# Performance work log

Hardware: AMD Instinct MI355X
Metric: run time of the kernel (lower is better)

## Reference

```python
import jax, jax.numpy as jnp
import numpy as np

N, D = 65536, 64            # flattened batch, state dim (size_in)
G, K = 4, 512               # number of gammas, components per gamma


def setup_inputs() -> dict:
    key = jax.random.key(0)
    k1, k2 = jax.random.split(key)
    states = jax.random.normal(k1, (N, D), dtype=jnp.float32)
    centers = jax.random.normal(k2, (G, K, D), dtype=jnp.float32)  # RBF centers, one bank per gamma
    gammas = jnp.array([0.5, 1.0, 2.0, 5.0], dtype=jnp.float32)
    return {"states": states, "centers": centers, "gammas": gammas}


def reference(states, centers, gammas):
    # states: [N, D]; centers: [G, K, D]; gammas: [G]
    x2 = jnp.sum(states * states, axis=-1)            # [N]
    c2 = jnp.sum(centers * centers, axis=-1)          # [G, K]
    xc = jnp.einsum('nd,gkd->gnk', states, centers)   # [G, N, K]
    d2 = x2[None, :, None] + c2[:, None, :] - 2.0 * xc  # [G, N, K]
    d2 = jnp.maximum(d2, 0.0)
    feats = jnp.exp(-gammas[:, None, None] * d2)      # [G, N, K]
    # concatenate per-gamma feature banks along feature dim -> [N, G*K]
    out = jnp.moveaxis(feats, 0, 1).reshape(states.shape[0], -1)
    return out
```

## Files before the change

kernel.cpp:

```cpp
#include <hip/hip_runtime.h>
#include <math.h>

#define N_TOT 65536
#define D_DIM 64
#define G_NUM 4
#define K_NUM 512

typedef __attribute__((ext_vector_type(4))) float  f32x4;
typedef __attribute__((ext_vector_type(8))) short  short8;

typedef const __attribute__((address_space(1))) void glb_cv;
typedef __attribute__((address_space(3))) void lds_v;

__device__ __forceinline__ unsigned int f2u(float x)        { return __builtin_bit_cast(unsigned int, x); }
__device__ __forceinline__ float        u2f(unsigned int x) { return __builtin_bit_cast(float, x); }

__device__ __forceinline__ unsigned int bf_rne(float x) {
    unsigned int u = f2u(x);
    return (u + 0x7FFFu + ((u >> 16) & 1u)) >> 16;
}

__device__ __forceinline__ int swz(int row, int byteInRow) {
    return (row << 7) + (byteInRow ^ ((row & 7) << 4));
}

#define AHI_OFF 0
#define ALO_OFF 16384
#define BHI_OFF 32768
#define BLO_OFF 49152

__global__ void prep_kernel(const float* __restrict__ in,
                            unsigned char* __restrict__ tiles,
                            float* __restrict__ sq, int nrows)
{
    int gtid = blockIdx.x * 256 + threadIdx.x;
    if (gtid >= nrows * 8) return;
    int row = gtid >> 3, c = gtid & 7;
    const float* p = in + (size_t)row * D_DIM + 8 * c;
    float4 v0 = *(const float4*)p;
    float4 v1 = *(const float4*)(p + 4);
    float vs[8] = {v0.x, v0.y, v0.z, v0.w, v1.x, v1.y, v1.z, v1.w};
    unsigned hi[4], lo[4];
    float s = 0.f;
    #pragma unroll
    for (int i = 0; i < 4; ++i) {
        float a = vs[2 * i], b = vs[2 * i + 1];
        s += a * a + b * b;
        unsigned ha = f2u(a) & 0xFFFF0000u, hb = f2u(b) & 0xFFFF0000u;
        hi[i] = (ha >> 16) | hb;
        lo[i] = bf_rne(a - u2f(ha)) | (bf_rne(b - u2f(hb)) << 16);
    }
    int tile = row >> 7, r = row & 127;
    int cs = c ^ (r & 7);
    unsigned char* base = tiles + (size_t)tile * 32768 + r * 128 + cs * 16;
    *(uint4*)(base)         = make_uint4(hi[0], hi[1], hi[2], hi[3]);
    *(uint4*)(base + 16384) = make_uint4(lo[0], lo[1], lo[2], lo[3]);
    s += __shfl_xor(s, 1, 64);
    s += __shfl_xor(s, 2, 64);
    s += __shfl_xor(s, 4, 64);
    if (c == 0) sq[row] = s;
}

__global__ __launch_bounds__(256, 2)
void rbf_mfma2(const unsigned char* __restrict__ Aprep,
               const unsigned char* __restrict__ Bprep,
               const float* __restrict__ gammas,
               const float* __restrict__ x2,
               const float* __restrict__ c2,
               float* __restrict__ out)
{
    __shared__ __align__(16) unsigned char lds[65536];

    const int tid = threadIdx.x;
    const int n0  = blockIdx.x * 128;
    const int kt  = blockIdx.y;
    const int g   = blockIdx.z;
    const int k0  = kt * 128;

    const int lane = tid & 63;
    const int w    = tid >> 6;

    const unsigned char* Asrc = Aprep + (size_t)blockIdx.x * 32768;
    const unsigned char* Bsrc = Bprep + (size_t)(g * 4 + kt) * 32768;
    #pragma unroll
    for (int i = 0; i < 8; ++i) {
        const int off = w * 8192 + i * 1024;
        __builtin_amdgcn_global_load_lds((glb_cv*)(Asrc + off + lane * 16),
                                         (lds_v*)(lds + off), 16, 0, 0);
        __builtin_amdgcn_global_load_lds((glb_cv*)(Bsrc + off + lane * 16),
                                         (lds_v*)(lds + 32768 + off), 16, 0, 0);
    }
    __syncthreads();

    const int wr = w >> 1;
    const int wc = w & 1;
    const int fr = lane & 15;
    const int q  = lane >> 4;

    short8 xhi[4][2], xlo[4][2];
    #pragma unroll
    for (int ms = 0; ms < 4; ++ms) {
        const int row = wr * 64 + ms * 16 + fr;
        #pragma unroll
        for (int h = 0; h < 2; ++h) {
            const int off = swz(row, 64 * h + 16 * q);
            xhi[ms][h] = *(const short8*)(lds + AHI_OFF + off);
            xlo[ms][h] = *(const short8*)(lds + ALO_OFF + off);
        }
    }

    f32x4 acc[4][4];
    #pragma unroll
    for (int ms = 0; ms < 4; ++ms)
        #pragma unroll
        for (int ns = 0; ns < 4; ++ns)
            acc[ms][ns] = (f32x4){0.f, 0.f, 0.f, 0.f};

    #pragma unroll
    for (int ns = 0; ns < 4; ++ns) {
        const int rowc = wc * 64 + ns * 16 + fr;
        short8 chi[2], clo[2];
        #pragma unroll
        for (int h = 0; h < 2; ++h) {
            const int off = swz(rowc, 64 * h + 16 * q);
            chi[h] = *(const short8*)(lds + BHI_OFF + off);
            clo[h] = *(const short8*)(lds + BLO_OFF + off);
        }
        #pragma unroll
        for (int ms = 0; ms < 4; ++ms) {
            #pragma unroll
            for (int h = 0; h < 2; ++h) {
                acc[ms][ns] = __builtin_amdgcn_mfma_f32_16x16x32_bf16(chi[h], xhi[ms][h], acc[ms][ns], 0, 0, 0);
                acc[ms][ns] = __builtin_amdgcn_mfma_f32_16x16x32_bf16(chi[h], xlo[ms][h], acc[ms][ns], 0, 0, 0);
                acc[ms][ns] = __builtin_amdgcn_mfma_f32_16x16x32_bf16(clo[h], xhi[ms][h], acc[ms][ns], 0, 0, 0);
            }
        }
    }

    const float gamma = gammas[g];

    float c2v[4][4];
    const float* c2g = c2 + g * K_NUM + k0 + wc * 64;
    #pragma unroll
    for (int ns = 0; ns < 4; ++ns) {
        float4 t = *(const float4*)(c2g + ns * 16 + 4 * q);
        c2v[ns][0] = t.x; c2v[ns][1] = t.y; c2v[ns][2] = t.z; c2v[ns][3] = t.w;
    }

    #pragma unroll
    for (int ms = 0; ms < 4; ++ms) {
        const int n = n0 + wr * 64 + ms * 16 + fr;
        const float xv = x2[n];
        float* rowp = out + (size_t)n * (G_NUM * K_NUM) + (size_t)g * K_NUM + k0 + wc * 64;
        #pragma unroll
        for (int ns = 0; ns < 4; ++ns) {
            float4 o;
            o.x = __expf(-gamma * fmaxf(xv + c2v[ns][0] - 2.0f * acc[ms][ns][0], 0.f));
            o.y = __expf(-gamma * fmaxf(xv + c2v[ns][1] - 2.0f * acc[ms][ns][1], 0.f));
            o.z = __expf(-gamma * fmaxf(xv + c2v[ns][2] - 2.0f * acc[ms][ns][2], 0.f));
            o.w = __expf(-gamma * fmaxf(xv + c2v[ns][3] - 2.0f * acc[ms][ns][3], 0.f));
            *(float4*)(rowp + ns * 16 + 4 * q) = o;
        }
    }
}

extern "C" void kernel_launch(void* const* d_in, const int* in_sizes, int n_in,
                              void* d_out, int out_size, void* d_ws, size_t ws_size,
                              hipStream_t stream) {
    const float* states  = (const float*)d_in[0];
    const float* centers = (const float*)d_in[1];
    const float* gammas  = (const float*)d_in[2];
    float* out = (float*)d_out;

    unsigned char* Aprep = (unsigned char*)d_ws;
    unsigned char* Bprep = Aprep + (size_t)512 * 32768;
    float* x2 = (float*)(Bprep + (size_t)16 * 32768);
    float* c2 = x2 + N_TOT;

    prep_kernel<<<(N_TOT * 8) / 256, 256, 0, stream>>>(states, Aprep, x2, N_TOT);
    prep_kernel<<<(G_NUM * K_NUM * 8) / 256, 256, 0, stream>>>(centers, Bprep, c2, G_NUM * K_NUM);

    dim3 grid(N_TOT / 128, K_NUM / 128, G_NUM);
    rbf_mfma2<<<grid, 256, 0, stream>>>(Aprep, Bprep, gammas, x2, c2, out);
}
```

Measured before the change: 589.5 us.

## Persist A tile per block and loop over all B tiles with double-buffered prefetch

Each block now holds a 256-row slice of the prepped states in LDS and iterates over all 16 gamma/k center tiles, prefetching the next B tile into a second LDS buffer while computing the current one. This removes redundant reloading of state tiles across the previous 3D grid and overlaps center loads with MFMA work. It uses 128 KB of LDS and 512-thread blocks, which reduces occupancy and yields only 256 blocks total.

```diff
diff --git a/kernel.cpp b/kernel.cpp
--- a/kernel.cpp
+++ b/kernel.cpp
@@ -5,6 +5,7 @@
 #define D_DIM 64
 #define G_NUM 4
 #define K_NUM 512
+#define RB    256
 
 typedef __attribute__((ext_vector_type(4))) float  f32x4;
 typedef __attribute__((ext_vector_type(8))) short  short8;
@@ -23,11 +24,6 @@
 __device__ __forceinline__ int swz(int row, int byteInRow) {
     return (row << 7) + (byteInRow ^ ((row & 7) << 4));
 }
-
-#define AHI_OFF 0
-#define ALO_OFF 16384
-#define BHI_OFF 32768
-#define BLO_OFF 49152
 
 __global__ void prep_kernel(const float* __restrict__ in,
                             unsigned char* __restrict__ tiles,
@@ -61,106 +57,134 @@
     if (c == 0) sq[row] = s;
 }
 
-__global__ __launch_bounds__(256, 2)
-void rbf_mfma2(const unsigned char* __restrict__ Aprep,
+__global__ __launch_bounds__(512, 2)
+void rbf_mfma3(const unsigned char* __restrict__ Aprep,
                const unsigned char* __restrict__ Bprep,
                const float* __restrict__ gammas,
                const float* __restrict__ x2,
                const float* __restrict__ c2,
                float* __restrict__ out)
 {
-    __shared__ __align__(16) unsigned char lds[65536];
-
-    const int tid = threadIdx.x;
-    const int n0  = blockIdx.x * 128;
-    const int kt  = blockIdx.y;
-    const int g   = blockIdx.z;
-    const int k0  = kt * 128;
-
+    __shared__ __align__(16) unsigned char lds[131072];
+
+    const int tid  = threadIdx.x;
     const int lane = tid & 63;
     const int w    = tid >> 6;
-
-    const unsigned char* Asrc = Aprep + (size_t)blockIdx.x * 32768;
-    const unsigned char* Bsrc = Bprep + (size_t)(g * 4 + kt) * 32768;
+    const int n0   = blockIdx.x * RB;
+
+    const unsigned char* Asrc = Aprep + (size_t)blockIdx.x * 65536;
     #pragma unroll
     for (int i = 0; i < 8; ++i) {
-        const int off = w * 8192 + i * 1024;
+        const int off = i * 8192 + w * 1024;
         __builtin_amdgcn_global_load_lds((glb_cv*)(Asrc + off + lane * 16),
                                          (lds_v*)(lds + off), 16, 0, 0);
-        __builtin_amdgcn_global_load_lds((glb_cv*)(Bsrc + off + lane * 16),
-                                         (lds_v*)(lds + 32768 + off), 16, 0, 0);
+    }
+    #pragma unroll
+    for (int i = 0; i < 4; ++i) {
+        const int off = i * 8192 + w * 1024;
+        __builtin_amdgcn_global_load_lds((glb_cv*)(Bprep + off + lane * 16),
+                                         (lds_v*)(lds + 65536 + off), 16, 0, 0);
     }
     __syncthreads();
 
-    const int wr = w >> 1;
-    const int wc = w & 1;
-    const int fr = lane & 15;
-    const int q  = lane >> 4;
+    const int wrow = w >> 1;
+    const int wcol = w & 1;
+    const int fr   = lane & 15;
+    const int q    = lane >> 4;
 
     short8 xhi[4][2], xlo[4][2];
     #pragma unroll
     for (int ms = 0; ms < 4; ++ms) {
-        const int row = wr * 64 + ms * 16 + fr;
+        const int row = wrow * 64 + ms * 16 + fr;
+        const int base = (row >> 7) * 32768;
         #pragma unroll
         for (int h = 0; h < 2; ++h) {
-            const int off = swz(row, 64 * h + 16 * q);
-            xhi[ms][h] = *(const short8*)(lds + AHI_OFF + off);
-            xlo[ms][h] = *(const short8*)(lds + ALO_OFF + off);
-        }
-    }
-
-    f32x4 acc[4][4];
+            const int off = base + swz(row & 127, 64 * h + 16 * q);
+            xhi[ms][h] = *(const short8*)(lds + off);
+            xlo[ms][h] = *(const short8*)(lds + off + 16384);
+        }
+    }
+
+    float x2v[4];
     #pragma unroll
     for (int ms = 0; ms < 4; ++ms)
-        #pragma unroll
-        for (int ns = 0; ns < 4; ++ns)
-            acc[ms][ns] = (f32x4){0.f, 0.f, 0.f, 0.f};
-
-    #pragma unroll
-    for (int ns = 0; ns < 4; ++ns) {
-        const int rowc = wc * 64 + ns * 16 + fr;
-        short8 chi[2], clo[2];
-        #pragma unroll
-        for (int h = 0; h < 2; ++h) {
-            const int off = swz(rowc, 64 * h + 16 * q);
-            chi[h] = *(const short8*)(lds + BHI_OFF + off);
-            clo[h] = *(const short8*)(lds + BLO_OFF + off);
-        }
+        x2v[ms] = x2[n0 + wrow * 64 + ms * 16 + fr];
+
+    const float4 gm = *(const float4*)gammas;
+
+    #pragma unroll 1
+    for (int t = 0; t < 16; ++t) {
+        const int g  = t >> 2;
+        const int kt = t & 3;
+        const int bb = 65536 + (t & 1) * 32768;
+
+        if (t < 15) {
+            const unsigned char* Bsrc = Bprep + (size_t)(t + 1) * 32768;
+            const int dstb = 65536 + ((t + 1) & 1) * 32768;
+            #pragma unroll
+            for (int i = 0; i < 4; ++i) {
+                const int off = i * 8192 + w * 1024;
+                __builtin_amdgcn_global_load_lds((glb_cv*)(Bsrc + off + lane * 16),
+                                                 (lds_v*)(lds + dstb + off), 16, 0, 0);
+            }
+        }
+
+        f32x4 acc[4][4];
+        #pragma unroll
+        for (int ms = 0; ms < 4; ++ms)
+            #pragma unroll
+            for (int ns = 0; ns < 4; ++ns)
+                acc[ms][ns] = (f32x4){0.f, 0.f, 0.f, 0.f};
+
+        #pragma unroll
+        for (int ns = 0; ns < 4; ++ns) {
+            const int rowc = wcol * 64 + ns * 16 + fr;
+            short8 chi[2], clo[2];
+            #pragma unroll
+            for (int h = 0; h < 2; ++h) {
+                const int off = bb + swz(rowc, 64 * h + 16 * q);
+                chi[h] = *(const short8*)(lds + off);
+                clo[h] = *(const short8*)(lds + off + 16384);
+            }
+            #pragma unroll
+            for (int ms = 0; ms < 4; ++ms) {
+                #pragma unroll
+                for (int h = 0; h < 2; ++h) {
+                    acc[ms][ns] = __builtin_amdgcn_mfma_f32_16x16x32_bf16(chi[h], xhi[ms][h], acc[ms][ns], 0, 0, 0);
+                    acc[ms][ns] = __builtin_amdgcn_mfma_f32_16x16x32_bf16(chi[h], xlo[ms][h], acc[ms][ns], 0, 0, 0);
+                    acc[ms][ns] = __builtin_amdgcn_mfma_f32_16x16x32_bf16(clo[h], xhi[ms][h], acc[ms][ns], 0, 0, 0);
+                }
+            }
+        }
+
+        const float gamma = (g == 0) ? gm.x : (g == 1) ? gm.y : (g == 2) ? gm.z : gm.w;
+        const int   col0  = g * K_NUM + kt * 128 + wcol * 64;
+
+        float c2v[4][4];
+        const float* c2g = c2 + col0;
+        #pragma unroll
+        for (int ns = 0; ns < 4; ++ns) {
+            float4 tt = *(const float4*)(c2g + ns * 16 + 4 * q);
+            c2v[ns][0] = tt.x; c2v[ns][1] = tt.y; c2v[ns][2] = tt.z; c2v[ns][3] = tt.w;
+        }
+
         #pragma unroll
         for (int ms = 0; ms < 4; ++ms) {
-            #pragma unroll
-            for (int h = 0; h < 2; ++h) {
-                acc[ms][ns] = __builtin_amdgcn_mfma_f32_16x16x32_bf16(chi[h], xhi[ms][h], acc[ms][ns], 0, 0, 0);
-                acc[ms][ns] = __builtin_amdgcn_mfma_f32_16x16x32_bf16(chi[h], xlo[ms][h], acc[ms][ns], 0, 0, 0);
-                acc[ms][ns] = __builtin_amdgcn_mfma_f32_16x16x32_bf16(clo[h], xhi[ms][h], acc[ms][ns], 0, 0, 0);
-            }
-        }
-    }
-
-    const float gamma = gammas[g];
-
-    float c2v[4][4];
-    const float* c2g = c2 + g * K_NUM + k0 + wc * 64;
-    #pragma unroll
-    for (int ns = 0; ns < 4; ++ns) {
-        float4 t = *(const float4*)(c2g + ns * 16 + 4 * q);
-        c2v[ns][0] = t.x; c2v[ns][1] = t.y; c2v[ns][2] = t.z; c2v[ns][3] = t.w;
-    }
-
-    #pragma unroll
-    for (int ms = 0; ms < 4; ++ms) {
-        const int n = n0 + wr * 64 + ms * 16 + fr;
-        const float xv = x2[n];
-        float* rowp = out + (size_t)n * (G_NUM * K_NUM) + (size_t)g * K_NUM + k0 + wc * 64;
-        #pragma unroll
-        for (int ns = 0; ns < 4; ++ns) {
-            float4 o;
-            o.x = __expf(-gamma * fmaxf(xv + c2v[ns][0] - 2.0f * acc[ms][ns][0], 0.f));
-            o.y = __expf(-gamma * fmaxf(xv + c2v[ns][1] - 2.0f * acc[ms][ns][1], 0.f));
-            o.z = __expf(-gamma * fmaxf(xv + c2v[ns][2] - 2.0f * acc[ms][ns][2], 0.f));
-            o.w = __expf(-gamma * fmaxf(xv + c2v[ns][3] - 2.0f * acc[ms][ns][3], 0.f));
-            *(float4*)(rowp + ns * 16 + 4 * q) = o;
-        }
+            const int n = n0 + wrow * 64 + ms * 16 + fr;
+            const float xv = x2v[ms];
+            float* rowp = out + (size_t)n * (G_NUM * K_NUM) + col0;
+            #pragma unroll
+            for (int ns = 0; ns < 4; ++ns) {
+                float4 o;
+                o.x = __expf(-gamma * fmaxf(xv + c2v[ns][0] - 2.0f * acc[ms][ns][0], 0.f));
+                o.y = __expf(-gamma * fmaxf(xv + c2v[ns][1] - 2.0f * acc[ms][ns][1], 0.f));
+                o.z = __expf(-gamma * fmaxf(xv + c2v[ns][2] - 2.0f * acc[ms][ns][2], 0.f));
+                o.w = __expf(-gamma * fmaxf(xv + c2v[ns][3] - 2.0f * acc[ms][ns][3], 0.f));
+                *(float4*)(rowp + ns * 16 + 4 * q) = o;
+            }
+        }
+
+        __syncthreads();
     }
 }
 
@@ -180,6 +204,5 @@
     prep_kernel<<<(N_TOT * 8) / 256, 256, 0, stream>>>(states, Aprep, x2, N_TOT);
     prep_kernel<<<(G_NUM * K_NUM * 8) / 256, 256, 0, stream>>>(centers, Bprep, c2, G_NUM * K_NUM);
 
-    dim3 grid(N_TOT / 128, K_NUM / 128, G_NUM);
-    rbf_mfma2<<<grid, 256, 0, stream>>>(Aprep, Bprep, gammas, x2, c2, out);
-}
+    rbf_mfma3<<<dim3(N_TOT / RB), 512, 0, stream>>>(Aprep, Bprep, gammas, x2, c2, out);
+}
```

New measurement: 571.7 us. 3.0% less time.
